# Kernel tuning notes

Hardware: AMD Instinct MI355X
Metric: run time of the kernel (lower is better)

## Reference

```python
import jax, jax.numpy as jnp
import numpy as np

B, CIN, X, Y, Z = 4, 1, 64, 64, 64
W = 32          # fno_layer_size
L = 6           # num_fno_layers
M = 32          # modes per axis
CLIFT = CIN + 3 # coord features appended


def setup_inputs() -> dict:
    key = jax.random.key(0)
    ks = jax.random.split(key, 16)
    scale = 1.0 / (W * W)
    inp = {
        "x": jax.random.normal(ks[0], (B, CIN, X, Y, Z), dtype=jnp.float32),
        # lift network (two 1x1 conv3d layers)
        "lw1": jax.random.normal(ks[1], (W // 2, CLIFT), dtype=jnp.float32) * 0.1,
        "lb1": jnp.zeros((W // 2,), dtype=jnp.float32),
        "lw2": jax.random.normal(ks[2], (W, W // 2), dtype=jnp.float32) * 0.1,
        "lb2": jnp.zeros((W,), dtype=jnp.float32),
        # factorized spectral weights per layer: [L, in, out, modes, 2]
        "wx": jax.random.uniform(ks[3], (L, W, W, M, 2), dtype=jnp.float32) * scale,
        "wy": jax.random.uniform(ks[4], (L, W, W, M, 2), dtype=jnp.float32) * scale,
        "wz": jax.random.uniform(ks[5], (L, W, W, M, 2), dtype=jnp.float32) * scale,
        # per-layer MLP (1x1 conv3d: W -> 2W -> W)
        "mw1": jax.random.normal(ks[6], (L, 2 * W, W), dtype=jnp.float32) * 0.1,
        "mb1": jnp.zeros((L, 2 * W), dtype=jnp.float32),
        "mw2": jax.random.normal(ks[7], (L, W, 2 * W), dtype=jnp.float32) * 0.1,
        "mb2": jnp.zeros((L, W), dtype=jnp.float32),
    }
    return inp


def _pw(x, w, b):
    # 1x1x1 conv3d == per-voxel channel matmul
    return jnp.einsum('bixyz,oi->boxyz', x, w) + b[None, :, None, None, None]


def _spectral(x, wx, wy, wz):
    # x: [B, C, X, Y, Z]; wx/wy/wz: [C, C, M, 2] real -> complex
    cx = wx[..., 0] + 1j * wx[..., 1]
    cy = wy[..., 0] + 1j * wy[..., 1]
    cz = wz[..., 0] + 1j * wz[..., 1]
    _, _, sx, sy, sz = x.shape
    # z axis
    xf = jnp.fft.rfft(x, axis=-1, norm='ortho')
    oz = jnp.einsum('bixyz,ioz->boxyz', xf[..., :M], cz)
    oz = jnp.pad(oz, [(0, 0)] * 4 + [(0, sz // 2 + 1 - M)])
    out = jnp.fft.irfft(oz, n=sz, axis=-1, norm='ortho')
    # y axis
    xf = jnp.fft.rfft(x, axis=-2, norm='ortho')
    oy = jnp.einsum('bixyz,ioy->boxyz', xf[:, :, :, :M, :], cy)
    oy = jnp.pad(oy, [(0, 0)] * 3 + [(0, sy // 2 + 1 - M), (0, 0)])
    out = out + jnp.fft.irfft(oy, n=sy, axis=-2, norm='ortho')
    # x axis
    xf = jnp.fft.rfft(x, axis=-3, norm='ortho')
    ox = jnp.einsum('bixyz,iox->boxyz', xf[:, :, :M, :, :], cx)
    ox = jnp.pad(ox, [(0, 0)] * 2 + [(0, sx // 2 + 1 - M), (0, 0), (0, 0)])
    out = out + jnp.fft.irfft(ox, n=sx, axis=-3, norm='ortho')
    return out


def _meshgrid(b, sx, sy, sz, dtype):
    gx = jnp.linspace(0.0, 1.0, sx, dtype=dtype)
    gy = jnp.linspace(0.0, 1.0, sy, dtype=dtype)
    gz = jnp.linspace(0.0, 1.0, sz, dtype=dtype)
    GX, GY, GZ = jnp.meshgrid(gx, gy, gz, indexing='ij')
    g = jnp.stack([GX, GY, GZ], axis=0)            # [3, X, Y, Z]
    return jnp.broadcast_to(g[None], (b, 3, sx, sy, sz))


def reference(x, lw1, lb1, lw2, lb2, wx, wy, wz, mw1, mb1, mw2, mb2):
    b = x.shape[0]
    coord = _meshgrid(b, X, Y, Z, x.dtype)
    h = jnp.concatenate([x, coord], axis=1)         # [B, CIN+3, X, Y, Z]
    h = _pw(h, lw1, lb1)
    h = jax.nn.gelu(h, approximate=False)
    h = _pw(h, lw2, lb2)
    for l in range(L):
        s = _spectral(h, wx[l], wy[l], wz[l])
        s = _pw(s, mw1[l], mb1[l])
        s = jax.nn.gelu(s, approximate=False)
        s = _pw(s, mw2[l], mb2[l])
        h = s + h
    return h
```

## Files before the change

### kernel.cpp

```cpp
#include <hip/hip_runtime.h>
#include <math.h>


#define BB 4
#define CC 32
#define NN 64
#define MM 32
#define NSITE 8
#define STH 512

__global__ __launch_bounds__(256) void lift_kernel(
    const float* __restrict__ x,
    const float* __restrict__ lw1, const float* __restrict__ lb1,
    const float* __restrict__ lw2, const float* __restrict__ lb2,
    float* __restrict__ h)
{
    __shared__ float w1[64], b1s[16], w2[512], b2s[32];
    int tid = threadIdx.x;
    if (tid < 64) w1[tid] = lw1[tid];
    if (tid < 16) b1s[tid] = lb1[tid];
    for (int i = tid; i < 512; i += 256) w2[i] = lw2[i];
    if (tid < 32) b2s[tid] = lb2[tid];
    __syncthreads();

    int v = blockIdx.x * 256 + tid;
    int b = v >> 18;
    int vox = v & 262143;
    float feat0 = x[b * 262144 + vox];
    float feat1 = (float)(vox >> 12)        * (1.0f / 63.0f);
    float feat2 = (float)((vox >> 6) & 63)  * (1.0f / 63.0f);
    float feat3 = (float)(vox & 63)         * (1.0f / 63.0f);

    float t1[16];
#pragma unroll
    for (int o = 0; o < 16; ++o) {
        float a = b1s[o];
        a = fmaf(w1[o * 4 + 0], feat0, a);
        a = fmaf(w1[o * 4 + 1], feat1, a);
        a = fmaf(w1[o * 4 + 2], feat2, a);
        a = fmaf(w1[o * 4 + 3], feat3, a);
        t1[o] = 0.5f * a * (1.0f + erff(a * 0.70710678118654752f));
    }
    int base = b * CC * 262144 + vox;
#pragma unroll
    for (int c = 0; c < 32; ++c) {
        float a = b2s[c];
#pragma unroll
        for (int o = 0; o < 16; ++o) a = fmaf(w2[c * 16 + o], t1[o], a);
        h[base + c * 262144] = a;
    }
}

template <int AXIS, bool ACCUM>
__global__ __launch_bounds__(STH) void spectral_kernel(
    const float* __restrict__ h, float* __restrict__ sout,
    const float2* __restrict__ w)
{
    __shared__ float lds[34176];
    float*  xm    = lds;
    float2* mspec = (float2*)lds;
    float2* spec  = (float2*)(lds + 16896);
    float*  ybuf  = lds + 16896;
    float2* roots = (float2*)(lds + 34048);

    const int tid = threadIdx.x;
    const int site0 = blockIdx.x * NSITE;
    const int b  = site0 >> 12;
    const int q0 = site0 & 4095;

    if (tid < 64) {
        float ss, sc;
        sincosf((float)tid * (6.283185307179586f / 64.0f), &ss, &sc);
        roots[tid] = make_float2(sc, ss);
    }

#pragma unroll
    for (int k = 0; k < 32; ++k) {
        int e = tid + k * STH;
        int c, s, t;
        if (AXIS == 2) { t = e & 63; s = (e >> 6) & 7; c = e >> 9; }
        else           { s = e & 7;  t = (e >> 3) & 63; c = e >> 9; }
        int q = q0 + s;
        int addr;
        if (AXIS == 2)      addr = (b * CC + c) * 262144 + q * 64 + t;
        else if (AXIS == 1) addr = (b * CC + c) * 262144 + (q >> 6) * 4096 + t * 64 + (q & 63);
        else                addr = (b * CC + c) * 262144 + t * 4096 + (q >> 6) * 64 + (q & 63);
        xm[(c * NSITE + s) * 66 + t] = h[addr];
    }
    __syncthreads();

    {
        const int mt = tid & 7;
        const int lt = tid >> 3;
        const int m0 = mt * 4;
        float ar[4][4], ai[4][4];
#pragma unroll
        for (int j = 0; j < 4; ++j) {
            float x0  = xm[(lt * 4 + j) * 66 + 0];
            float x32 = xm[(lt * 4 + j) * 66 + 32];
#pragma unroll
            for (int i = 0; i < 4; ++i) {
                ar[j][i] = (i & 1) ? (x0 - x32) : (x0 + x32);
                ai[j][i] = 0.0f;
            }
        }
        int idx0 = m0 + 0, idx1 = m0 + 1, idx2 = m0 + 2, idx3 = m0 + 3;
        for (int t = 1; t < 32; ++t) {
            float p[4], q[4];
#pragma unroll
            for (int j = 0; j < 4; ++j) {
                float xa = xm[(lt * 4 + j) * 66 + t];
                float xb = xm[(lt * 4 + j) * 66 + 64 - t];
                p[j] = xa + xb;
                q[j] = xa - xb;
            }
            float2 r0 = roots[idx0], r1 = roots[idx1], r2 = roots[idx2], r3 = roots[idx3];
            idx0 = (idx0 + m0 + 0) & 63;
            idx1 = (idx1 + m0 + 1) & 63;
            idx2 = (idx2 + m0 + 2) & 63;
            idx3 = (idx3 + m0 + 3) & 63;
#pragma unroll
            for (int j = 0; j < 4; ++j) {
                ar[j][0] = fmaf(p[j], r0.x, ar[j][0]); ai[j][0] = fmaf(-q[j], r0.y, ai[j][0]);
                ar[j][1] = fmaf(p[j], r1.x, ar[j][1]); ai[j][1] = fmaf(-q[j], r1.y, ai[j][1]);
                ar[j][2] = fmaf(p[j], r2.x, ar[j][2]); ai[j][2] = fmaf(-q[j], r2.y, ai[j][2]);
                ar[j][3] = fmaf(p[j], r3.x, ar[j][3]); ai[j][3] = fmaf(-q[j], r3.y, ai[j][3]);
            }
        }
#pragma unroll
        for (int j = 0; j < 4; ++j) {
            int line = lt * 4 + j;
            int c = line >> 3, s = line & 7;
#pragma unroll
            for (int i = 0; i < 4; ++i)
                spec[(s * CC + c) * MM + m0 + i] =
                    make_float2(ar[j][i] * 0.125f, ai[j][i] * 0.125f);
        }
    }
    __syncthreads();

    {
        const int m  = tid & 31;
        const int st = (tid >> 5) & 1;
        const int ot = tid >> 6;
        float ar[4][4], ai[4][4];
#pragma unroll
        for (int js = 0; js < 4; ++js)
#pragma unroll
            for (int jo = 0; jo < 4; ++jo) { ar[js][jo] = 0.0f; ai[js][jo] = 0.0f; }
        for (int i = 0; i < CC; ++i) {
            float2 sv[4];
#pragma unroll
            for (int js = 0; js < 4; ++js) sv[js] = spec[((st * 4 + js) * CC + i) * MM + m];
#pragma unroll
            for (int jo = 0; jo < 4; ++jo) {
                float2 wv = w[(i * CC + ot * 4 + jo) * MM + m];
#pragma unroll
                for (int js = 0; js < 4; ++js) {
                    ar[js][jo] = fmaf(sv[js].x, wv.x, fmaf(-sv[js].y, wv.y, ar[js][jo]));
                    ai[js][jo] = fmaf(sv[js].x, wv.y, fmaf( sv[js].y, wv.x, ai[js][jo]));
                }
            }
        }
        __syncthreads();
#pragma unroll
        for (int js = 0; js < 4; ++js) {
            int s = st * 4 + js;
#pragma unroll
            for (int jo = 0; jo < 4; ++jo) {
                int o = ot * 4 + jo;
                mspec[(o * NSITE + s) * 33 + m] = make_float2(ar[js][jo], ai[js][jo]);
            }
        }
    }
    __syncthreads();

    {
        const int tt = tid & 7;
        const int lt = tid >> 3;
        float u[4][4], vv[4][4], wsum[4], m0r[4];
#pragma unroll
        for (int j = 0; j < 4; ++j) {
            m0r[j] = mspec[(lt * 4 + j) * 33].x;
            wsum[j] = 0.0f;
#pragma unroll
            for (int jj = 0; jj < 4; ++jj) { u[j][jj] = 0.5f * m0r[j]; vv[j][jj] = 0.0f; }
        }
        const int p0 = tt * 4 + 1, p1 = tt * 4 + 2, p2 = tt * 4 + 3, p3 = tt * 4 + 4;
        int i0 = p0, i1 = p1, i2 = p2, i3 = p3;
        for (int m = 1; m < 32; ++m) {
            float2 sv[4];
#pragma unroll
            for (int j = 0; j < 4; ++j) sv[j] = mspec[(lt * 4 + j) * 33 + m];
            float2 r0 = roots[i0], r1 = roots[i1], r2 = roots[i2], r3 = roots[i3];
            i0 = (i0 + p0) & 63;
            i1 = (i1 + p1) & 63;
            i2 = (i2 + p2) & 63;
            i3 = (i3 + p3) & 63;
#pragma unroll
            for (int j = 0; j < 4; ++j) {
                u[j][0] = fmaf(sv[j].x, r0.x, u[j][0]); vv[j][0] = fmaf(sv[j].y, r0.y, vv[j][0]);
                u[j][1] = fmaf(sv[j].x, r1.x, u[j][1]); vv[j][1] = fmaf(sv[j].y, r1.y, vv[j][1]);
                u[j][2] = fmaf(sv[j].x, r2.x, u[j][2]); vv[j][2] = fmaf(sv[j].y, r2.y, vv[j][2]);
                u[j][3] = fmaf(sv[j].x, r3.x, u[j][3]); vv[j][3] = fmaf(sv[j].y, r3.y, vv[j][3]);
                wsum[j] += sv[j].x;
            }
        }
#pragma unroll
        for (int j = 0; j < 4; ++j) {
            int line = lt * 4 + j;
            ybuf[line * 67 + p0]               = (u[j][0] - vv[j][0]) * 0.25f;
            ybuf[line * 67 + ((64 - p0) & 63)] = (u[j][0] + vv[j][0]) * 0.25f;
            ybuf[line * 67 + p1]               = (u[j][1] - vv[j][1]) * 0.25f;
            ybuf[line * 67 + ((64 - p1) & 63)] = (u[j][1] + vv[j][1]) * 0.25f;
            ybuf[line * 67 + p2]               = (u[j][2] - vv[j][2]) * 0.25f;
            ybuf[line * 67 + ((64 - p2) & 63)] = (u[j][2] + vv[j][2]) * 0.25f;
            ybuf[line * 67 + p3]               = (u[j][3] - vv[j][3]) * 0.25f;
            ybuf[line * 67 + ((64 - p3) & 63)] = (u[j][3] + vv[j][3]) * 0.25f;
            if (tt == 0)
                ybuf[line * 67 + 0] = (0.5f * m0r[j] + wsum[j]) * 0.25f;
        }
    }
    __syncthreads();

#pragma unroll
    for (int k = 0; k < 32; ++k) {
        int e = tid + k * STH;
        int o, s, t;
        if (AXIS == 2) { t = e & 63; s = (e >> 6) & 7; o = e >> 9; }
        else           { s = e & 7;  t = (e >> 3) & 63; o = e >> 9; }
        int q = q0 + s;
        int addr;
        if (AXIS == 2)      addr = (b * CC + o) * 262144 + q * 64 + t;
        else if (AXIS == 1) addr = (b * CC + o) * 262144 + (q >> 6) * 4096 + t * 64 + (q & 63);
        else                addr = (b * CC + o) * 262144 + t * 4096 + (q >> 6) * 64 + (q & 63);
        float v = ybuf[(o * NSITE + s) * 67 + t];
        if (ACCUM) sout[addr] += v;
        else       sout[addr] = v;
    }
}

__global__ __launch_bounds__(256) void mlp_kernel(
    const float* __restrict__ sin_, float* __restrict__ hio,
    const float* __restrict__ mw1, const float* __restrict__ mb1,
    const float* __restrict__ mw2, const float* __restrict__ mb2)
{
    const float4* w1v = (const float4*)mw1;
    const float4* w2v = (const float4*)mw2;

    int tid = threadIdx.x;
    int v = blockIdx.x * 256 + tid;
    int b = v >> 18;
    int vox = v & 262143;
    int base = b * CC * 262144 + vox;

    float sv[32];
#pragma unroll
    for (int i = 0; i < 32; ++i) sv[i] = sin_[base + i * 262144];

    float acc[32];
#pragma unroll
    for (int c = 0; c < 32; ++c) acc[c] = mb2[c];

#pragma unroll
    for (int ch = 0; ch < 4; ++ch) {
        float t1c[16];
#pragma unroll
        for (int o16 = 0; o16 < 16; ++o16) {
            int o = ch * 16 + o16;
            float a = mb1[o];
#pragma unroll
            for (int i4 = 0; i4 < 8; ++i4) {
                float4 wv = w1v[o * 8 + i4];
                a = fmaf(wv.x, sv[i4 * 4 + 0], a);
                a = fmaf(wv.y, sv[i4 * 4 + 1], a);
                a = fmaf(wv.z, sv[i4 * 4 + 2], a);
                a = fmaf(wv.w, sv[i4 * 4 + 3], a);
            }
            t1c[o16] = 0.5f * a * (1.0f + erff(a * 0.70710678118654752f));
        }
#pragma unroll
        for (int c = 0; c < 32; ++c) {
#pragma unroll
            for (int o4 = 0; o4 < 4; ++o4) {
                float4 wv = w2v[c * 16 + ch * 4 + o4];
                acc[c] = fmaf(wv.x, t1c[o4 * 4 + 0], acc[c]);
                acc[c] = fmaf(wv.y, t1c[o4 * 4 + 1], acc[c]);
                acc[c] = fmaf(wv.z, t1c[o4 * 4 + 2], acc[c]);
                acc[c] = fmaf(wv.w, t1c[o4 * 4 + 3], acc[c]);
            }
        }
    }
#pragma unroll
    for (int c = 0; c < 32; ++c) hio[base + c * 262144] += acc[c];
}

extern "C" void kernel_launch(void* const* d_in, const int* in_sizes, int n_in,
                              void* d_out, int out_size, void* d_ws, size_t ws_size,
                              hipStream_t stream) {
    const float* x   = (const float*)d_in[0];
    const float* lw1 = (const float*)d_in[1];
    const float* lb1 = (const float*)d_in[2];
    const float* lw2 = (const float*)d_in[3];
    const float* lb2 = (const float*)d_in[4];
    const float* wx  = (const float*)d_in[5];
    const float* wy  = (const float*)d_in[6];
    const float* wz  = (const float*)d_in[7];
    const float* mw1 = (const float*)d_in[8];
    const float* mb1 = (const float*)d_in[9];
    const float* mw2 = (const float*)d_in[10];
    const float* mb2 = (const float*)d_in[11];

    float* h = (float*)d_out;
    float* s = (float*)d_ws;

    lift_kernel<<<4096, 256, 0, stream>>>(x, lw1, lb1, lw2, lb2, h);

    for (int l = 0; l < 6; ++l) {
        const float2* wxl = (const float2*)wx + l * 32768;
        const float2* wyl = (const float2*)wy + l * 32768;
        const float2* wzl = (const float2*)wz + l * 32768;
        spectral_kernel<2, false><<<2048, STH, 0, stream>>>(h, s, wzl);
        spectral_kernel<1, true ><<<2048, STH, 0, stream>>>(h, s, wyl);
        spectral_kernel<0, true ><<<2048, STH, 0, stream>>>(h, s, wxl);
        mlp_kernel<<<4096, 256, 0, stream>>>(s, h,
            mw1 + l * 2048, mb1 + l * 64, mw2 + l * 2048, mb2 + l * 32);
    }
}
```

Before: 10.51 ms.

## Fuse z-axis spectral convolution with per-layer MLP and residual update

The z-axis spectral pass now runs last in each layer, in a new kernel that also applies the two-layer pointwise MLP with GELU and the residual add. That kernel adds its spectral result from shared memory to the partial sum from the y and x passes, then updates h in place. This removes the separate MLP launch and one full write and read of the intermediate buffer per layer. The cost is that the register-heavy MLP now runs inside a block that holds a large LDS footprint, so occupancy during the MLP phase may be lower. The kernel also passes the same buffer through two restrict-qualified pointers.

After: 10.28 ms. 1.02x faster.

```diff
diff --git a/kernel.cpp b/kernel.cpp
--- a/kernel.cpp
+++ b/kernel.cpp
@@ -51,44 +51,16 @@
     }
 }
 
-template <int AXIS, bool ACCUM>
-__global__ __launch_bounds__(STH) void spectral_kernel(
-    const float* __restrict__ h, float* __restrict__ sout,
-    const float2* __restrict__ w)
-{
-    __shared__ float lds[34176];
+
+__device__ __forceinline__ void spectral_core(
+    float* lds, int tid)
+{
     float*  xm    = lds;
     float2* mspec = (float2*)lds;
     float2* spec  = (float2*)(lds + 16896);
     float*  ybuf  = lds + 16896;
     float2* roots = (float2*)(lds + 34048);
 
-    const int tid = threadIdx.x;
-    const int site0 = blockIdx.x * NSITE;
-    const int b  = site0 >> 12;
-    const int q0 = site0 & 4095;
-
-    if (tid < 64) {
-        float ss, sc;
-        sincosf((float)tid * (6.283185307179586f / 64.0f), &ss, &sc);
-        roots[tid] = make_float2(sc, ss);
-    }
-
-#pragma unroll
-    for (int k = 0; k < 32; ++k) {
-        int e = tid + k * STH;
-        int c, s, t;
-        if (AXIS == 2) { t = e & 63; s = (e >> 6) & 7; c = e >> 9; }
-        else           { s = e & 7;  t = (e >> 3) & 63; c = e >> 9; }
-        int q = q0 + s;
-        int addr;
-        if (AXIS == 2)      addr = (b * CC + c) * 262144 + q * 64 + t;
-        else if (AXIS == 1) addr = (b * CC + c) * 262144 + (q >> 6) * 4096 + t * 64 + (q & 63);
-        else                addr = (b * CC + c) * 262144 + t * 4096 + (q >> 6) * 64 + (q & 63);
-        xm[(c * NSITE + s) * 66 + t] = h[addr];
-    }
-    __syncthreads();
-
     {
         const int mt = tid & 7;
         const int lt = tid >> 3;
@@ -138,6 +110,15 @@
         }
     }
     __syncthreads();
+}
+
+__device__ __forceinline__ void spectral_mix_inv(
+    float* lds, int tid, const float2* __restrict__ w)
+{
+    float2* mspec = (float2*)lds;
+    float2* spec  = (float2*)(lds + 16896);
+    float*  ybuf  = lds + 16896;
+    float2* roots = (float2*)(lds + 34048);
 
     {
         const int m  = tid & 31;
@@ -222,77 +203,143 @@
         }
     }
     __syncthreads();
+}
+
+template <int AXIS, bool ACCUM>
+__global__ __launch_bounds__(STH) void spectral_kernel(
+    const float* __restrict__ h, float* __restrict__ sout,
+    const float2* __restrict__ w)
+{
+    __shared__ float lds[34176];
+    float*  xm    = lds;
+    float*  ybuf  = lds + 16896;
+    float2* roots = (float2*)(lds + 34048);
+
+    const int tid = threadIdx.x;
+    const int site0 = blockIdx.x * NSITE;
+    const int b  = site0 >> 12;
+    const int q0 = site0 & 4095;
+
+    if (tid < 64) {
+        float ss, sc;
+        sincosf((float)tid * (6.283185307179586f / 64.0f), &ss, &sc);
+        roots[tid] = make_float2(sc, ss);
+    }
 
 #pragma unroll
     for (int k = 0; k < 32; ++k) {
         int e = tid + k * STH;
-        int o, s, t;
-        if (AXIS == 2) { t = e & 63; s = (e >> 6) & 7; o = e >> 9; }
-        else           { s = e & 7;  t = (e >> 3) & 63; o = e >> 9; }
+        int s = e & 7, t = (e >> 3) & 63, c = e >> 9;
         int q = q0 + s;
         int addr;
-        if (AXIS == 2)      addr = (b * CC + o) * 262144 + q * 64 + t;
-        else if (AXIS == 1) addr = (b * CC + o) * 262144 + (q >> 6) * 4096 + t * 64 + (q & 63);
-        else                addr = (b * CC + o) * 262144 + t * 4096 + (q >> 6) * 64 + (q & 63);
+        if (AXIS == 1) addr = (b * CC + c) * 262144 + (q >> 6) * 4096 + t * 64 + (q & 63);
+        else           addr = (b * CC + c) * 262144 + t * 4096 + (q >> 6) * 64 + (q & 63);
+        xm[(c * NSITE + s) * 66 + t] = h[addr];
+    }
+    __syncthreads();
+
+    spectral_core(lds, tid);
+    spectral_mix_inv(lds, tid, w);
+
+#pragma unroll
+    for (int k = 0; k < 32; ++k) {
+        int e = tid + k * STH;
+        int s = e & 7, t = (e >> 3) & 63, o = e >> 9;
+        int q = q0 + s;
+        int addr;
+        if (AXIS == 1) addr = (b * CC + o) * 262144 + (q >> 6) * 4096 + t * 64 + (q & 63);
+        else           addr = (b * CC + o) * 262144 + t * 4096 + (q >> 6) * 64 + (q & 63);
         float v = ybuf[(o * NSITE + s) * 67 + t];
         if (ACCUM) sout[addr] += v;
         else       sout[addr] = v;
     }
 }
 
-__global__ __launch_bounds__(256) void mlp_kernel(
-    const float* __restrict__ sin_, float* __restrict__ hio,
+__global__ __launch_bounds__(STH) void spectral_mlp_z_kernel(
+    const float* __restrict__ hin, float* __restrict__ hio,
+    const float* __restrict__ s_in,
+    const float2* __restrict__ w,
     const float* __restrict__ mw1, const float* __restrict__ mb1,
     const float* __restrict__ mw2, const float* __restrict__ mb2)
 {
-    const float4* w1v = (const float4*)mw1;
-    const float4* w2v = (const float4*)mw2;
-
-    int tid = threadIdx.x;
-    int v = blockIdx.x * 256 + tid;
-    int b = v >> 18;
-    int vox = v & 262143;
-    int base = b * CC * 262144 + vox;
-
-    float sv[32];
-#pragma unroll
-    for (int i = 0; i < 32; ++i) sv[i] = sin_[base + i * 262144];
-
-    float acc[32];
-#pragma unroll
-    for (int c = 0; c < 32; ++c) acc[c] = mb2[c];
-
-#pragma unroll
-    for (int ch = 0; ch < 4; ++ch) {
-        float t1c[16];
-#pragma unroll
-        for (int o16 = 0; o16 < 16; ++o16) {
-            int o = ch * 16 + o16;
-            float a = mb1[o];
-#pragma unroll
-            for (int i4 = 0; i4 < 8; ++i4) {
-                float4 wv = w1v[o * 8 + i4];
-                a = fmaf(wv.x, sv[i4 * 4 + 0], a);
-                a = fmaf(wv.y, sv[i4 * 4 + 1], a);
-                a = fmaf(wv.z, sv[i4 * 4 + 2], a);
-                a = fmaf(wv.w, sv[i4 * 4 + 3], a);
-            }
-            t1c[o16] = 0.5f * a * (1.0f + erff(a * 0.70710678118654752f));
-        }
-#pragma unroll
-        for (int c = 0; c < 32; ++c) {
-#pragma unroll
-            for (int o4 = 0; o4 < 4; ++o4) {
-                float4 wv = w2v[c * 16 + ch * 4 + o4];
-                acc[c] = fmaf(wv.x, t1c[o4 * 4 + 0], acc[c]);
-                acc[c] = fmaf(wv.y, t1c[o4 * 4 + 1], acc[c]);
-                acc[c] = fmaf(wv.z, t1c[o4 * 4 + 2], acc[c]);
-                acc[c] = fmaf(wv.w, t1c[o4 * 4 + 3], acc[c]);
-            }
-        }
-    }
-#pragma unroll
-    for (int c = 0; c < 32; ++c) hio[base + c * 262144] += acc[c];
+    __shared__ float lds[34176];
+    float*  xm    = lds;
+    float*  ybuf  = lds + 16896;
+    float2* roots = (float2*)(lds + 34048);
+
+    const int tid = threadIdx.x;
+    const int site0 = blockIdx.x * NSITE;
+    const int b  = site0 >> 12;
+    const int q0 = site0 & 4095;
+
+    if (tid < 64) {
+        float ss, sc;
+        sincosf((float)tid * (6.283185307179586f / 64.0f), &ss, &sc);
+        roots[tid] = make_float2(sc, ss);
+    }
+
+#pragma unroll
+    for (int k = 0; k < 32; ++k) {
+        int e = tid + k * STH;
+        int t = e & 63, s = (e >> 6) & 7, c = e >> 9;
+        int q = q0 + s;
+        xm[(c * NSITE + s) * 66 + t] = hin[(b * CC + c) * 262144 + q * 64 + t];
+    }
+    __syncthreads();
+
+    spectral_core(lds, tid);
+    spectral_mix_inv(lds, tid, w);
+
+    {
+        const int s = tid >> 6;
+        const int t = tid & 63;
+        const int q = q0 + s;
+        const int g = (b * CC) * 262144 + q * 64 + t;
+
+        const float4* w1v = (const float4*)mw1;
+        const float4* w2v = (const float4*)mw2;
+
+        float out[32];
+#pragma unroll
+        for (int c = 0; c < 32; ++c)
+            out[c] = ybuf[(c * NSITE + s) * 67 + t] + s_in[g + c * 262144];
+
+        float acc[32];
+#pragma unroll
+        for (int c = 0; c < 32; ++c) acc[c] = mb2[c];
+
+#pragma unroll
+        for (int ch = 0; ch < 4; ++ch) {
+            float t1c[16];
+#pragma unroll
+            for (int o16 = 0; o16 < 16; ++o16) {
+                int o = ch * 16 + o16;
+                float a = mb1[o];
+#pragma unroll
+                for (int i4 = 0; i4 < 8; ++i4) {
+                    float4 wv = w1v[o * 8 + i4];
+                    a = fmaf(wv.x, out[i4 * 4 + 0], a);
+                    a = fmaf(wv.y, out[i4 * 4 + 1], a);
+                    a = fmaf(wv.z, out[i4 * 4 + 2], a);
+                    a = fmaf(wv.w, out[i4 * 4 + 3], a);
+                }
+                t1c[o16] = 0.5f * a * (1.0f + erff(a * 0.70710678118654752f));
+            }
+#pragma unroll
+            for (int c = 0; c < 32; ++c) {
+#pragma unroll
+                for (int o4 = 0; o4 < 4; ++o4) {
+                    float4 wv = w2v[c * 16 + ch * 4 + o4];
+                    acc[c] = fmaf(wv.x, t1c[o4 * 4 + 0], acc[c]);
+                    acc[c] = fmaf(wv.y, t1c[o4 * 4 + 1], acc[c]);
+                    acc[c] = fmaf(wv.z, t1c[o4 * 4 + 2], acc[c]);
+                    acc[c] = fmaf(wv.w, t1c[o4 * 4 + 3], acc[c]);
+                }
+            }
+        }
+#pragma unroll
+        for (int c = 0; c < 32; ++c) hio[g + c * 262144] += acc[c];
+    }
 }
 
 extern "C" void kernel_launch(void* const* d_in, const int* in_sizes, int n_in,
@@ -320,10 +367,9 @@
         const float2* wxl = (const float2*)wx + l * 32768;
         const float2* wyl = (const float2*)wy + l * 32768;
         const float2* wzl = (const float2*)wz + l * 32768;
-        spectral_kernel<2, false><<<2048, STH, 0, stream>>>(h, s, wzl);
-        spectral_kernel<1, true ><<<2048, STH, 0, stream>>>(h, s, wyl);
+        spectral_kernel<1, false><<<2048, STH, 0, stream>>>(h, s, wyl);
         spectral_kernel<0, true ><<<2048, STH, 0, stream>>>(h, s, wxl);
-        mlp_kernel<<<4096, 256, 0, stream>>>(s, h,
+        spectral_mlp_z_kernel<<<2048, STH, 0, stream>>>(h, h, s, wzl,
             mw1 + l * 2048, mb1 + l * 64, mw2 + l * 2048, mb2 + l * 32);
     }
 }
```
